# Kernel tuning notes

Measured on AMD Instinct MI355X. Metric: run time of the kernel, lower is better.

## Reference

```python
import jax, jax.numpy as jnp
import numpy as np

B, N, D = 8, 256, 128
EPS_AGG = 1e-6
LN_EPS = 1e-5


def setup_inputs() -> dict:
    key = jax.random.key(0)
    ks = jax.random.split(key, 12)
    s = lambda fan_in: 1.0 / np.sqrt(fan_in)
    inp = {
        "x": jax.random.normal(ks[0], (B, N, D), dtype=jnp.float32),
        "edge0": jax.random.normal(ks[1], (B, N, N, D), dtype=jnp.float32),
        "edge_mask": jax.random.randint(ks[2], (B, N, N), 0, 2, dtype=jnp.int32),
        # msg_mlp: Linear(3D->D), ReLU, Linear(D->D)
        "W1m": jax.random.uniform(ks[3], (3 * D, D), jnp.float32, -s(3 * D), s(3 * D)),
        "b1m": jax.random.uniform(ks[4], (D,), jnp.float32, -s(3 * D), s(3 * D)),
        "W2m": jax.random.uniform(ks[5], (D, D), jnp.float32, -s(D), s(D)),
        "b2m": jax.random.uniform(ks[6], (D,), jnp.float32, -s(D), s(D)),
        # upd_mlp: Linear(2D->D), ReLU, Linear(D->D)
        "W1u": jax.random.uniform(ks[7], (2 * D, D), jnp.float32, -s(2 * D), s(2 * D)),
        "b1u": jax.random.uniform(ks[8], (D,), jnp.float32, -s(2 * D), s(2 * D)),
        "W2u": jax.random.uniform(ks[9], (D, D), jnp.float32, -s(D), s(D)),
        "b2u": jax.random.uniform(ks[10], (D,), jnp.float32, -s(D), s(D)),
        # LayerNorm affine
        "gamma": jnp.ones((D,), jnp.float32),
        "beta": jnp.zeros((D,), jnp.float32),
    }
    return inp


def reference(x, edge0, edge_mask, W1m, b1m, W2m, b2m, W1u, b1u, W2u, b2u, gamma, beta):
    # All-pairs concat: [B, N_i, N_j, 3D]
    xi = jnp.broadcast_to(x[:, :, None, :], (B, N, N, D))
    xj = jnp.broadcast_to(x[:, None, :, :], (B, N, N, D))
    msg_in = jnp.concatenate([xi, xj, edge0], axis=-1)
    # 2-layer edge MLP
    h = jax.nn.relu(jnp.einsum("bijk,kd->bijd", msg_in, W1m) + b1m)
    msg = jnp.einsum("bijk,kd->bijd", h, W2m) + b2m
    # mask + mean-style aggregation over neighbors j
    m = edge_mask.astype(jnp.float32)
    agg = jnp.einsum("bijd,bij->bid", msg, m) / (m.sum(axis=2, keepdims=True) + EPS_AGG)
    # update MLP
    u_in = jnp.concatenate([x, agg], axis=-1)  # [B, N, 2D]
    hu = jax.nn.relu(u_in @ W1u + b1u)
    out = hu @ W2u + b2u
    # residual + LayerNorm
    y = x + out
    mu = y.mean(axis=-1, keepdims=True)
    var = y.var(axis=-1, keepdims=True)
    return (y - mu) * jax.lax.rsqrt(var + LN_EPS) * gamma + beta
```

## Files before the change

kernel.cpp:

```cpp
#include <hip/hip_runtime.h>
#include <hip/hip_bf16.h>

typedef float    f4    __attribute__((ext_vector_type(4)));
typedef short    s8v   __attribute__((ext_vector_type(8)));
typedef __bf16   bf8v  __attribute__((ext_vector_type(8)));
typedef unsigned int u32x4v __attribute__((ext_vector_type(4)));
typedef unsigned short u16;

typedef const __attribute__((address_space(1))) void GAS;
typedef __attribute__((address_space(3))) void LAS;

#define NB 8
#define NN 256
#define ND 128

static __device__ __forceinline__ u16 f2bf(float f) {
    union { float f; unsigned u; } v; v.f = f;
    unsigned r = v.u + 0x7FFF + ((v.u >> 16) & 1);
    return (u16)(r >> 16);
}

static __device__ __forceinline__ unsigned pack2bf(float a, float b) {
    unsigned ua = __builtin_bit_cast(unsigned, a) + 0x8000u;
    unsigned ub = __builtin_bit_cast(unsigned, b) + 0x8000u;
    return __builtin_amdgcn_perm(ub, ua, 0x07060302u);
}

__global__ __launch_bounds__(256) void prep_kernel(
    const float* __restrict__ x, const float* __restrict__ W1m,
    const float* __restrict__ b1m,
    float* __restrict__ P, float* __restrict__ Qt, u16* __restrict__ W1cp)
{
    if (blockIdx.x == 1024) {
        for (int idx = threadIdx.x; idx < 16384; idx += 256) {
            int e  = idx & 7;
            int ln = (idx >> 3) & 63;
            int nt = (idx >> 9) & 7;
            int kt = idx >> 12;
            int k  = kt * 32 + (ln >> 4) * 8 + e;
            int d  = nt * 16 + (ln & 15);
            W1cp[idx] = f2bf(W1m[(2 * ND + k) * ND + d]);
        }
        return;
    }
    __shared__ float xl[256];
    int t = threadIdx.x;
    int row0 = blockIdx.x * 2;
    xl[t] = x[row0 * ND + t];
    __syncthreads();
    int r = t >> 7;
    int d = t & 127;
    int row = row0 + r;
    float sp = b1m[d], sq = 0.f;
    const float* xr = &xl[r * ND];
    #pragma unroll 8
    for (int k = 0; k < ND; ++k) {
        float xv = xr[k];
        sp += xv * W1m[k * ND + d];
        sq += xv * W1m[(ND + k) * ND + d];
    }
    P[row * ND + d] = sp;
    Qt[((size_t)((row >> 8) * ND + d)) * NN + (row & 255)] = sq;
}

__global__ __launch_bounds__(256, 4) void fused_kernel(
    const float* __restrict__ x, const float* __restrict__ edge0,
    const int* __restrict__ mask,
    const float* __restrict__ W2m, const float* __restrict__ b2m,
    const float* __restrict__ W1u, const float* __restrict__ b1u,
    const float* __restrict__ W2u, const float* __restrict__ b2u,
    const float* __restrict__ gamma, const float* __restrict__ beta,
    const float* __restrict__ P, const float* __restrict__ Qt,
    const u16* __restrict__ W1cp,
    float* __restrict__ out)
{
    __shared__ float ebuf[2][32 * 128];
    __shared__ float ml[NN];
    __shared__ float aggH[ND];
    __shared__ float xrow[ND];
    __shared__ float am[ND];
    __shared__ float hu[ND];
    __shared__ float yl[ND];
    __shared__ float redc[4], redA[4], redB[4];

    const int bid  = blockIdx.x;
    const int b    = bid >> 8;
    const int tid  = threadIdx.x;
    const int wave = tid >> 6;
    const int lane = tid & 63;
    const int l15  = lane & 15;
    const int lg   = lane >> 4;

    const char* e0c = (const char*)(edge0 + (size_t)bid * (NN * ND));

    float mval = (float)mask[bid * NN + tid];
    ml[tid] = mval;
    if (tid < ND) xrow[tid] = x[bid * ND + tid];

    s8v bfr[4][2];
    #pragma unroll
    for (int kt = 0; kt < 4; ++kt)
        #pragma unroll
        for (int n = 0; n < 2; ++n)
            bfr[kt][n] = *reinterpret_cast<const s8v*>(
                &W1cp[(((kt * 8) + (wave * 2 + n)) * 64 + lane) * 8]);

    const int col0 = wave * 32 + l15;
    const float pv0 = P[bid * ND + col0];
    const float pv1 = P[bid * ND + col0 + 16];
    const float* qt0 = Qt + (size_t)(b * ND + col0) * NN;
    const float* qt1 = qt0 + (size_t)16 * NN;

    auto STAGE = [&](int cc, int bb) {
        const char* cb = e0c + (size_t)cc * 16384;
        #pragma unroll
        for (int u = 0; u < 4; ++u) {
            int row  = wave * 8 + u * 2 + (lane >> 5);
            int colb = (lane & 31) * 16;
            const char* g = cb + row * 512 + (colb ^ ((row & 7) << 4));
            __builtin_amdgcn_global_load_lds(
                (GAS*)g, (LAS*)&ebuf[bb][(wave * 4 + u) * 256], 16, 0, 0);
        }
    };

    float agg0 = 0.f, agg1 = 0.f;
    f4 q0r[2][2], q1r[2][2];

    #pragma unroll
    for (int m = 0; m < 2; ++m) {
        int j0 = m * 16 + lg * 4;
        q0r[0][m] = *reinterpret_cast<const f4*>(qt0 + j0);
        q1r[0][m] = *reinterpret_cast<const f4*>(qt1 + j0);
    }
    __builtin_amdgcn_sched_barrier(0);
    STAGE(0, 0);
    __builtin_amdgcn_sched_barrier(0);

    #pragma unroll
    for (int c = 0; c < 8; ++c) {
        const int pb = c & 1, nb = pb ^ 1;
        if (c < 7) {
            #pragma unroll
            for (int m = 0; m < 2; ++m) {
                int j0 = (c + 1) * 32 + m * 16 + lg * 4;
                q0r[nb][m] = *reinterpret_cast<const f4*>(qt0 + j0);
                q1r[nb][m] = *reinterpret_cast<const f4*>(qt1 + j0);
            }
            __builtin_amdgcn_sched_barrier(0);
            STAGE(c + 1, nb);
            __builtin_amdgcn_sched_barrier(0);
            asm volatile("s_waitcnt vmcnt(8) lgkmcnt(0)" ::: "memory");
        } else {
            asm volatile("s_waitcnt vmcnt(0) lgkmcnt(0)" ::: "memory");
        }
        __builtin_amdgcn_s_barrier();
        __builtin_amdgcn_sched_barrier(0);

        const char* bufc = (const char*)&ebuf[pb][0];
        #pragma unroll
        for (int m = 0; m < 2; ++m) {
            f4 acc0 = {0.f, 0.f, 0.f, 0.f};
            f4 acc1 = {0.f, 0.f, 0.f, 0.f};
            int row = m * 16 + l15;
            int rb  = row * 512;
            int swz = (row & 7) << 4;
            #pragma unroll
            for (int kt = 0; kt < 4; ++kt) {
                int cbyte = kt * 128 + lg * 32;
                f4 a0 = *reinterpret_cast<const f4*>(bufc + rb + ((cbyte)      ^ swz));
                f4 a1 = *reinterpret_cast<const f4*>(bufc + rb + ((cbyte + 16) ^ swz));
                u32x4v aw;
                aw[0] = pack2bf(a0[0], a0[1]);
                aw[1] = pack2bf(a0[2], a0[3]);
                aw[2] = pack2bf(a1[0], a1[1]);
                aw[3] = pack2bf(a1[2], a1[3]);
                bf8v av = __builtin_bit_cast(bf8v, aw);
                acc0 = __builtin_amdgcn_mfma_f32_16x16x32_bf16(
                    av, __builtin_bit_cast(bf8v, bfr[kt][0]), acc0, 0, 0, 0);
                acc1 = __builtin_amdgcn_mfma_f32_16x16x32_bf16(
                    av, __builtin_bit_cast(bf8v, bfr[kt][1]), acc1, 0, 0, 0);
            }
            int j0 = c * 32 + m * 16 + lg * 4;
            f4 q0 = q0r[pb][m];
            f4 q1 = q1r[pb][m];
            #pragma unroll
            for (int r = 0; r < 4; ++r) {
                float mm = ml[j0 + r];
                float h0 = fmaxf(acc0[r] + pv0 + q0[r], 0.f);
                float h1 = fmaxf(acc1[r] + pv1 + q1[r], 0.f);
                agg0 += mm * h0;
                agg1 += mm * h1;
            }
        }
        __builtin_amdgcn_sched_barrier(0);
        __builtin_amdgcn_s_barrier();
    }

    agg0 += __shfl_xor(agg0, 16); agg0 += __shfl_xor(agg0, 32);
    agg1 += __shfl_xor(agg1, 16); agg1 += __shfl_xor(agg1, 32);
    if (lg == 0) {
        aggH[wave * 32 + l15]      = agg0;
        aggH[wave * 32 + 16 + l15] = agg1;
    }
    float cv = mval;
    #pragma unroll
    for (int o = 32; o > 0; o >>= 1) cv += __shfl_xor(cv, o);
    if (lane == 0) redc[wave] = cv;
    __syncthreads();

    const float cnt = redc[0] + redc[1] + redc[2] + redc[3];
    const float inv = 1.f / (cnt + 1e-6f);
    const int d  = tid & 127;
    const int hf = tid >> 7;

    {
        float s = 0.f;
        #pragma unroll 8
        for (int k = hf * 64; k < hf * 64 + 64; ++k) s += aggH[k] * W2m[k * ND + d];
        ml[tid] = s;
    }
    __syncthreads();
    if (tid < ND) am[d] = (ml[d] + ml[d + ND] + cnt * b2m[d]) * inv;
    __syncthreads();
    {
        float s = 0.f;
        const float* W = W1u + (size_t)hf * ND * ND;
        const float* v = hf ? am : xrow;
        #pragma unroll 8
        for (int k = 0; k < ND; ++k) s += v[k] * W[k * ND + d];
        ml[tid] = s;
    }
    __syncthreads();
    if (tid < ND) hu[d] = fmaxf(ml[d] + ml[d + ND] + b1u[d], 0.f);
    __syncthreads();
    {
        float s = 0.f;
        #pragma unroll 8
        for (int k = hf * 64; k < hf * 64 + 64; ++k) s += hu[k] * W2u[k * ND + d];
        ml[tid] = s;
    }
    __syncthreads();
    if (tid < ND) yl[d] = xrow[d] + ml[d] + ml[d + ND] + b2u[d];
    __syncthreads();
    float yv = (tid < ND) ? yl[tid] : 0.f;
    float s1 = yv, s2 = yv * yv;
    #pragma unroll
    for (int o = 32; o > 0; o >>= 1) { s1 += __shfl_xor(s1, o); s2 += __shfl_xor(s2, o); }
    if (lane == 0) { redA[wave] = s1; redB[wave] = s2; }
    __syncthreads();
    if (tid < ND) {
        float mu  = (redA[0] + redA[1] + redA[2] + redA[3]) * (1.f / 128.f);
        float ex2 = (redB[0] + redB[1] + redB[2] + redB[3]) * (1.f / 128.f);
        float var = ex2 - mu * mu;
        float rs  = rsqrtf(var + 1e-5f);
        out[bid * ND + d] = (yl[d] - mu) * rs * gamma[d] + beta[d];
    }
}

extern "C" void kernel_launch(void* const* d_in, const int* in_sizes, int n_in,
                              void* d_out, int out_size, void* d_ws, size_t ws_size,
                              hipStream_t stream) {
    (void)in_sizes; (void)n_in; (void)out_size; (void)ws_size;
    const float* x     = (const float*)d_in[0];
    const float* edge0 = (const float*)d_in[1];
    const int*   mask  = (const int*)d_in[2];
    const float* W1m   = (const float*)d_in[3];
    const float* b1m   = (const float*)d_in[4];
    const float* W2m   = (const float*)d_in[5];
    const float* b2m   = (const float*)d_in[6];
    const float* W1u   = (const float*)d_in[7];
    const float* b1u   = (const float*)d_in[8];
    const float* W2u   = (const float*)d_in[9];
    const float* b2u   = (const float*)d_in[10];
    const float* gamma = (const float*)d_in[11];
    const float* beta  = (const float*)d_in[12];

    float* P    = (float*)d_ws;
    float* Qt   = P + 2048 * 128;
    u16*   W1cp = (u16*)(Qt + 8 * 128 * 256);

    float* o = (float*)d_out;

    prep_kernel<<<dim3(1025), dim3(256), 0, stream>>>(x, W1m, b1m, P, Qt, W1cp);
    fused_kernel<<<dim3(2048), dim3(256), 0, stream>>>(
        x, edge0, mask, W2m, b2m, W1u, b1u, W2u, b2u, gamma, beta,
        P, Qt, W1cp, o);
}
```

Before: 101.0 us.

## Triple-buffer edge staging and drop per-iteration trailing barrier

Switches the edge tile staging from double to triple buffering, prefetching two chunks ahead and issuing the next loads right after the top barrier. This removes the second block-wide barrier per iteration and deepens load latency hiding. Epilogue shared arrays are aliased onto the first staging buffer to limit LDS growth, and launch bounds are lowered to 3 blocks per CU to match the larger LDS footprint, trading occupancy for pipelining depth.

```diff
diff --git a/kernel.cpp b/kernel.cpp
--- a/kernel.cpp
+++ b/kernel.cpp
@@ -63,7 +63,7 @@
     Qt[((size_t)((row >> 8) * ND + d)) * NN + (row & 255)] = sq;
 }
 
-__global__ __launch_bounds__(256, 4) void fused_kernel(
+__global__ __launch_bounds__(256, 3) void fused_kernel(
     const float* __restrict__ x, const float* __restrict__ edge0,
     const int* __restrict__ mask,
     const float* __restrict__ W2m, const float* __restrict__ b2m,
@@ -74,14 +74,15 @@
     const u16* __restrict__ W1cp,
     float* __restrict__ out)
 {
-    __shared__ float ebuf[2][32 * 128];
+    __shared__ float ebuf[3][32 * 128];
     __shared__ float ml[NN];
-    __shared__ float aggH[ND];
     __shared__ float xrow[ND];
-    __shared__ float am[ND];
-    __shared__ float hu[ND];
-    __shared__ float yl[ND];
     __shared__ float redc[4], redA[4], redB[4];
+
+    float* aggH = &ebuf[0][0];
+    float* am   = &ebuf[0][128];
+    float* hu   = &ebuf[0][256];
+    float* yl   = &ebuf[0][384];
 
     const int bid  = blockIdx.x;
     const int b    = bid >> 8;
@@ -124,39 +125,42 @@
     };
 
     float agg0 = 0.f, agg1 = 0.f;
-    f4 q0r[2][2], q1r[2][2];
-
-    #pragma unroll
-    for (int m = 0; m < 2; ++m) {
-        int j0 = m * 16 + lg * 4;
-        q0r[0][m] = *reinterpret_cast<const f4*>(qt0 + j0);
-        q1r[0][m] = *reinterpret_cast<const f4*>(qt1 + j0);
-    }
+    f4 q0r[3][2], q1r[3][2];
+
+    auto LOADQ = [&](int cc, int gg) {
+        #pragma unroll
+        for (int m = 0; m < 2; ++m) {
+            int j0 = cc * 32 + m * 16 + lg * 4;
+            q0r[gg][m] = *reinterpret_cast<const f4*>(qt0 + j0);
+            q1r[gg][m] = *reinterpret_cast<const f4*>(qt1 + j0);
+        }
+    };
+
+    LOADQ(0, 0);
     __builtin_amdgcn_sched_barrier(0);
     STAGE(0, 0);
     __builtin_amdgcn_sched_barrier(0);
+    LOADQ(1, 1);
+    __builtin_amdgcn_sched_barrier(0);
+    STAGE(1, 1);
+    __builtin_amdgcn_sched_barrier(0);
 
     #pragma unroll
     for (int c = 0; c < 8; ++c) {
-        const int pb = c & 1, nb = pb ^ 1;
-        if (c < 7) {
-            #pragma unroll
-            for (int m = 0; m < 2; ++m) {
-                int j0 = (c + 1) * 32 + m * 16 + lg * 4;
-                q0r[nb][m] = *reinterpret_cast<const f4*>(qt0 + j0);
-                q1r[nb][m] = *reinterpret_cast<const f4*>(qt1 + j0);
-            }
-            __builtin_amdgcn_sched_barrier(0);
-            STAGE(c + 1, nb);
-            __builtin_amdgcn_sched_barrier(0);
+        const int g = c % 3;
+        if (c < 7)
             asm volatile("s_waitcnt vmcnt(8) lgkmcnt(0)" ::: "memory");
-        } else {
+        else
             asm volatile("s_waitcnt vmcnt(0) lgkmcnt(0)" ::: "memory");
-        }
         __builtin_amdgcn_s_barrier();
         __builtin_amdgcn_sched_barrier(0);
-
-        const char* bufc = (const char*)&ebuf[pb][0];
+        if (c < 6) {
+            LOADQ(c + 2, (c + 2) % 3);
+            __builtin_amdgcn_sched_barrier(0);
+            STAGE(c + 2, (c + 2) % 3);
+            __builtin_amdgcn_sched_barrier(0);
+        }
+        const char* bufc = (const char*)&ebuf[g][0];
         #pragma unroll
         for (int m = 0; m < 2; ++m) {
             f4 acc0 = {0.f, 0.f, 0.f, 0.f};
@@ -181,8 +185,8 @@
                     av, __builtin_bit_cast(bf8v, bfr[kt][1]), acc1, 0, 0, 0);
             }
             int j0 = c * 32 + m * 16 + lg * 4;
-            f4 q0 = q0r[pb][m];
-            f4 q1 = q1r[pb][m];
+            f4 q0 = q0r[g][m];
+            f4 q1 = q1r[g][m];
             #pragma unroll
             for (int r = 0; r < 4; ++r) {
                 float mm = ml[j0 + r];
@@ -192,8 +196,6 @@
                 agg1 += mm * h1;
             }
         }
-        __builtin_amdgcn_sched_barrier(0);
-        __builtin_amdgcn_s_barrier();
     }
 
     agg0 += __shfl_xor(agg0, 16); agg0 += __shfl_xor(agg0, 32);
```

Result: slower. 107.1 us (+6.0%).

## Compute xj projection via MFMA from staged bf16 x instead of precomputed Qt

Applied to the files above, without the earlier changes.

Drops the precomputed fp32 Qt (x_j·W1m middle block) and instead stages a bf16 copy of x alongside each edge tile in LDS, adding a second set of MFMAs per tile that multiply it by bf16 W1m weights. This removes the per-chunk Qt register loads and the scalar prep GEMM for Q, in exchange for doubling MFMA work and enlarging LDS. LDS is cut back by aliasing the small epilogue arrays into ebuf, and occupancy is lowered to 3 blocks. Block IDs are remapped so that consecutive blocks land in different batches, which spreads the xbf reads. The x_j term now runs in bf16 rather than fp32, so accuracy is slightly lower.

```diff
diff --git a/kernel.cpp b/kernel.cpp
--- a/kernel.cpp
+++ b/kernel.cpp
@@ -29,17 +29,20 @@
 __global__ __launch_bounds__(256) void prep_kernel(
     const float* __restrict__ x, const float* __restrict__ W1m,
     const float* __restrict__ b1m,
-    float* __restrict__ P, float* __restrict__ Qt, u16* __restrict__ W1cp)
+    float* __restrict__ P, u16* __restrict__ xbf_g, u16* __restrict__ W1cp)
 {
     if (blockIdx.x == 1024) {
-        for (int idx = threadIdx.x; idx < 16384; idx += 256) {
-            int e  = idx & 7;
-            int ln = (idx >> 3) & 63;
-            int nt = (idx >> 9) & 7;
-            int kt = idx >> 12;
+        for (int idx = threadIdx.x; idx < 32768; idx += 256) {
+            int half = idx >> 14;
+            int r  = idx & 16383;
+            int e  = r & 7;
+            int ln = (r >> 3) & 63;
+            int nt = (r >> 9) & 7;
+            int kt = r >> 12;
             int k  = kt * 32 + (ln >> 4) * 8 + e;
             int d  = nt * 16 + (ln & 15);
-            W1cp[idx] = f2bf(W1m[(2 * ND + k) * ND + d]);
+            int krow = half ? (ND + k) : (2 * ND + k);
+            W1cp[idx] = f2bf(W1m[krow * ND + d]);
         }
         return;
     }
@@ -51,39 +54,36 @@
     int r = t >> 7;
     int d = t & 127;
     int row = row0 + r;
-    float sp = b1m[d], sq = 0.f;
+    float sp = b1m[d];
     const float* xr = &xl[r * ND];
     #pragma unroll 8
-    for (int k = 0; k < ND; ++k) {
-        float xv = xr[k];
-        sp += xv * W1m[k * ND + d];
-        sq += xv * W1m[(ND + k) * ND + d];
-    }
+    for (int k = 0; k < ND; ++k) sp += xr[k] * W1m[k * ND + d];
     P[row * ND + d] = sp;
-    Qt[((size_t)((row >> 8) * ND + d)) * NN + (row & 255)] = sq;
-}
-
-__global__ __launch_bounds__(256, 4) void fused_kernel(
+    xbf_g[row * ND + d] = f2bf(xr[d]);
+}
+
+__global__ __launch_bounds__(256, 3) void fused_kernel(
     const float* __restrict__ x, const float* __restrict__ edge0,
     const int* __restrict__ mask,
     const float* __restrict__ W2m, const float* __restrict__ b2m,
     const float* __restrict__ W1u, const float* __restrict__ b1u,
     const float* __restrict__ W2u, const float* __restrict__ b2u,
     const float* __restrict__ gamma, const float* __restrict__ beta,
-    const float* __restrict__ P, const float* __restrict__ Qt,
+    const float* __restrict__ P, const u16* __restrict__ xbf_g,
     const u16* __restrict__ W1cp,
     float* __restrict__ out)
 {
-    __shared__ float ebuf[2][32 * 128];
+    __shared__ float ebuf[2][6144];
     __shared__ float ml[NN];
-    __shared__ float aggH[ND];
     __shared__ float xrow[ND];
-    __shared__ float am[ND];
-    __shared__ float hu[ND];
-    __shared__ float yl[ND];
     __shared__ float redc[4], redA[4], redB[4];
 
-    const int bid  = blockIdx.x;
+    float* aggH = &ebuf[0][0];
+    float* am   = &ebuf[0][128];
+    float* hu   = &ebuf[0][256];
+    float* yl   = &ebuf[0][384];
+
+    const int bid  = (blockIdx.x & 7) * 256 + (blockIdx.x >> 3);
     const int b    = bid >> 8;
     const int tid  = threadIdx.x;
     const int wave = tid >> 6;
@@ -92,24 +92,25 @@
     const int lg   = lane >> 4;
 
     const char* e0c = (const char*)(edge0 + (size_t)bid * (NN * ND));
+    const char* xbc = (const char*)(xbf_g + (size_t)b * NN * ND);
 
     float mval = (float)mask[bid * NN + tid];
     ml[tid] = mval;
     if (tid < ND) xrow[tid] = x[bid * ND + tid];
 
-    s8v bfr[4][2];
+    s8v bfrC[4][2], bfrB[4][2];
     #pragma unroll
     for (int kt = 0; kt < 4; ++kt)
         #pragma unroll
-        for (int n = 0; n < 2; ++n)
-            bfr[kt][n] = *reinterpret_cast<const s8v*>(
-                &W1cp[(((kt * 8) + (wave * 2 + n)) * 64 + lane) * 8]);
+        for (int n = 0; n < 2; ++n) {
+            int fo = (((kt * 8) + (wave * 2 + n)) * 64 + lane) * 8;
+            bfrC[kt][n] = *reinterpret_cast<const s8v*>(&W1cp[fo]);
+            bfrB[kt][n] = *reinterpret_cast<const s8v*>(&W1cp[16384 + fo]);
+        }
 
     const int col0 = wave * 32 + l15;
     const float pv0 = P[bid * ND + col0];
     const float pv1 = P[bid * ND + col0 + 16];
-    const float* qt0 = Qt + (size_t)(b * ND + col0) * NN;
-    const float* qt1 = qt0 + (size_t)16 * NN;
 
     auto STAGE = [&](int cc, int bb) {
         const char* cb = e0c + (size_t)cc * 16384;
@@ -121,18 +122,19 @@
             __builtin_amdgcn_global_load_lds(
                 (GAS*)g, (LAS*)&ebuf[bb][(wave * 4 + u) * 256], 16, 0, 0);
         }
+        const char* xb = xbc + (size_t)cc * 8192;
+        #pragma unroll
+        for (int u = 0; u < 2; ++u) {
+            int row  = wave * 8 + u * 4 + (lane >> 4);
+            int colb = (lane & 15) * 16;
+            const char* g = xb + row * 256 + (colb ^ ((row & 7) << 4));
+            __builtin_amdgcn_global_load_lds(
+                (GAS*)g, (LAS*)&ebuf[bb][4096 + (wave * 2 + u) * 256], 16, 0, 0);
+        }
     };
 
     float agg0 = 0.f, agg1 = 0.f;
-    f4 q0r[2][2], q1r[2][2];
-
-    #pragma unroll
-    for (int m = 0; m < 2; ++m) {
-        int j0 = m * 16 + lg * 4;
-        q0r[0][m] = *reinterpret_cast<const f4*>(qt0 + j0);
-        q1r[0][m] = *reinterpret_cast<const f4*>(qt1 + j0);
-    }
-    __builtin_amdgcn_sched_barrier(0);
+
     STAGE(0, 0);
     __builtin_amdgcn_sched_barrier(0);
 
@@ -140,16 +142,9 @@
     for (int c = 0; c < 8; ++c) {
         const int pb = c & 1, nb = pb ^ 1;
         if (c < 7) {
-            #pragma unroll
-            for (int m = 0; m < 2; ++m) {
-                int j0 = (c + 1) * 32 + m * 16 + lg * 4;
-                q0r[nb][m] = *reinterpret_cast<const f4*>(qt0 + j0);
-                q1r[nb][m] = *reinterpret_cast<const f4*>(qt1 + j0);
-            }
-            __builtin_amdgcn_sched_barrier(0);
             STAGE(c + 1, nb);
             __builtin_amdgcn_sched_barrier(0);
-            asm volatile("s_waitcnt vmcnt(8) lgkmcnt(0)" ::: "memory");
+            asm volatile("s_waitcnt vmcnt(6) lgkmcnt(0)" ::: "memory");
         } else {
             asm volatile("s_waitcnt vmcnt(0) lgkmcnt(0)" ::: "memory");
         }
@@ -176,18 +171,25 @@
                 aw[3] = pack2bf(a1[2], a1[3]);
                 bf8v av = __builtin_bit_cast(bf8v, aw);
                 acc0 = __builtin_amdgcn_mfma_f32_16x16x32_bf16(
-                    av, __builtin_bit_cast(bf8v, bfr[kt][0]), acc0, 0, 0, 0);
+                    av, __builtin_bit_cast(bf8v, bfrC[kt][0]), acc0, 0, 0, 0);
                 acc1 = __builtin_amdgcn_mfma_f32_16x16x32_bf16(
-                    av, __builtin_bit_cast(bf8v, bfr[kt][1]), acc1, 0, 0, 0);
+                    av, __builtin_bit_cast(bf8v, bfrC[kt][1]), acc1, 0, 0, 0);
+            }
+            #pragma unroll
+            for (int kt = 0; kt < 4; ++kt) {
+                int xoffb = 16384 + row * 256 + ((kt * 64 + lg * 16) ^ swz);
+                s8v xa = *reinterpret_cast<const s8v*>(bufc + xoffb);
+                acc0 = __builtin_amdgcn_mfma_f32_16x16x32_bf16(
+                    __builtin_bit_cast(bf8v, xa), __builtin_bit_cast(bf8v, bfrB[kt][0]), acc0, 0, 0, 0);
+                acc1 = __builtin_amdgcn_mfma_f32_16x16x32_bf16(
+                    __builtin_bit_cast(bf8v, xa), __builtin_bit_cast(bf8v, bfrB[kt][1]), acc1, 0, 0, 0);
             }
             int j0 = c * 32 + m * 16 + lg * 4;
-            f4 q0 = q0r[pb][m];
-            f4 q1 = q1r[pb][m];
             #pragma unroll
             for (int r = 0; r < 4; ++r) {
                 float mm = ml[j0 + r];
-                float h0 = fmaxf(acc0[r] + pv0 + q0[r], 0.f);
-                float h1 = fmaxf(acc1[r] + pv1 + q1[r], 0.f);
+                float h0 = fmaxf(acc0[r] + pv0, 0.f);
+                float h1 = fmaxf(acc1[r] + pv1, 0.f);
                 agg0 += mm * h0;
                 agg1 += mm * h1;
             }
@@ -276,13 +278,13 @@
     const float* beta  = (const float*)d_in[12];
 
     float* P    = (float*)d_ws;
-    float* Qt   = P + 2048 * 128;
-    u16*   W1cp = (u16*)(Qt + 8 * 128 * 256);
+    u16*   xbf  = (u16*)(P + 2048 * 128);
+    u16*   W1cp = xbf + 2048 * 128;
 
     float* o = (float*)d_out;
 
-    prep_kernel<<<dim3(1025), dim3(256), 0, stream>>>(x, W1m, b1m, P, Qt, W1cp);
+    prep_kernel<<<dim3(1025), dim3(256), 0, stream>>>(x, W1m, b1m, P, xbf, W1cp);
     fused_kernel<<<dim3(2048), dim3(256), 0, stream>>>(
         x, edge0, mask, W2m, b2m, W1u, b1u, W2u, b2u, gamma, beta,
-        P, Qt, W1cp, o);
-}
+        P, xbf, W1cp, o);
+}
```

Result: slower. 114.4 us (+13.2%).

## Split neighbor rows across waves with per-wave LDS buffers and full-width B fragments

Applied to the files above, without the earlier changes.

Each wave now owns 64 neighbor rows and computes all 128 output columns, holding the full W1 edge-slice B fragments (32 registers of 8 bf16) in registers. Each wave streams its own double-buffered LDS tile, so the per-chunk block barriers go away, and the A fragment is packed once and reused across 8 MFMA column tiles. The per-wave partial aggregates are then summed through LDS. Block indices are also remapped so consecutive blocks come from different batches, and launch bounds are lowered to 2 blocks per CU because register use and LDS use grow.

```diff
diff --git a/kernel.cpp b/kernel.cpp
--- a/kernel.cpp
+++ b/kernel.cpp
@@ -63,7 +63,7 @@
     Qt[((size_t)((row >> 8) * ND + d)) * NN + (row & 255)] = sq;
 }
 
-__global__ __launch_bounds__(256, 4) void fused_kernel(
+__global__ __launch_bounds__(256, 2) void fused_kernel(
     const float* __restrict__ x, const float* __restrict__ edge0,
     const int* __restrict__ mask,
     const float* __restrict__ W2m, const float* __restrict__ b2m,
@@ -74,16 +74,12 @@
     const u16* __restrict__ W1cp,
     float* __restrict__ out)
 {
-    __shared__ float ebuf[2][32 * 128];
+    __shared__ float ebuf[4][2][2048];
     __shared__ float ml[NN];
-    __shared__ float aggH[ND];
     __shared__ float xrow[ND];
-    __shared__ float am[ND];
-    __shared__ float hu[ND];
-    __shared__ float yl[ND];
     __shared__ float redc[4], redA[4], redB[4];
 
-    const int bid  = blockIdx.x;
+    const int bid  = (blockIdx.x & 7) * 256 + (blockIdx.x >> 3);
     const int b    = bid >> 8;
     const int tid  = threadIdx.x;
     const int wave = tid >> 6;
@@ -91,127 +87,123 @@
     const int l15  = lane & 15;
     const int lg   = lane >> 4;
 
-    const char* e0c = (const char*)(edge0 + (size_t)bid * (NN * ND));
+    const char* e0c = (const char*)(edge0 + (size_t)bid * (NN * ND))
+                    + (size_t)wave * 64 * 512;
 
     float mval = (float)mask[bid * NN + tid];
     ml[tid] = mval;
     if (tid < ND) xrow[tid] = x[bid * ND + tid];
 
-    s8v bfr[4][2];
+    s8v bfr[4][8];
     #pragma unroll
     for (int kt = 0; kt < 4; ++kt)
         #pragma unroll
-        for (int n = 0; n < 2; ++n)
-            bfr[kt][n] = *reinterpret_cast<const s8v*>(
-                &W1cp[(((kt * 8) + (wave * 2 + n)) * 64 + lane) * 8]);
-
-    const int col0 = wave * 32 + l15;
-    const float pv0 = P[bid * ND + col0];
-    const float pv1 = P[bid * ND + col0 + 16];
-    const float* qt0 = Qt + (size_t)(b * ND + col0) * NN;
-    const float* qt1 = qt0 + (size_t)16 * NN;
-
-    auto STAGE = [&](int cc, int bb) {
-        const char* cb = e0c + (size_t)cc * 16384;
-        #pragma unroll
-        for (int u = 0; u < 4; ++u) {
-            int row  = wave * 8 + u * 2 + (lane >> 5);
+        for (int nt = 0; nt < 8; ++nt)
+            bfr[kt][nt] = *reinterpret_cast<const s8v*>(
+                &W1cp[(((kt * 8) + nt) * 64 + lane) * 8]);
+
+    float pv[8];
+    #pragma unroll
+    for (int nt = 0; nt < 8; ++nt) pv[nt] = P[bid * ND + nt * 16 + l15];
+
+    const float* qb = Qt + ((size_t)b * ND + l15) * NN + wave * 64 + lg * 4;
+
+    float agg[8] = {0.f, 0.f, 0.f, 0.f, 0.f, 0.f, 0.f, 0.f};
+
+    auto STAGE = [&](int t, int bb) {
+        const char* cb = e0c + (size_t)t * 8192;
+        #pragma unroll
+        for (int u = 0; u < 8; ++u) {
+            int row  = u * 2 + (lane >> 5);
             int colb = (lane & 31) * 16;
             const char* g = cb + row * 512 + (colb ^ ((row & 7) << 4));
             __builtin_amdgcn_global_load_lds(
-                (GAS*)g, (LAS*)&ebuf[bb][(wave * 4 + u) * 256], 16, 0, 0);
+                (GAS*)g, (LAS*)&ebuf[wave][bb][u * 256], 16, 0, 0);
         }
     };
 
-    float agg0 = 0.f, agg1 = 0.f;
-    f4 q0r[2][2], q1r[2][2];
-
-    #pragma unroll
-    for (int m = 0; m < 2; ++m) {
-        int j0 = m * 16 + lg * 4;
-        q0r[0][m] = *reinterpret_cast<const f4*>(qt0 + j0);
-        q1r[0][m] = *reinterpret_cast<const f4*>(qt1 + j0);
-    }
+    asm volatile("s_waitcnt vmcnt(0) lgkmcnt(0)" ::: "memory");
     __builtin_amdgcn_sched_barrier(0);
     STAGE(0, 0);
     __builtin_amdgcn_sched_barrier(0);
 
     #pragma unroll
-    for (int c = 0; c < 8; ++c) {
-        const int pb = c & 1, nb = pb ^ 1;
-        if (c < 7) {
+    for (int t = 0; t < 4; ++t) {
+        const int pb = t & 1;
+        f4 qv[8];
+        #pragma unroll
+        for (int nt = 0; nt < 8; ++nt)
+            qv[nt] = *reinterpret_cast<const f4*>(qb + nt * 4096 + t * 16);
+        __builtin_amdgcn_sched_barrier(0);
+        if (t < 3) {
+            STAGE(t + 1, pb ^ 1);
+            __builtin_amdgcn_sched_barrier(0);
+            asm volatile("s_waitcnt vmcnt(8)" ::: "memory");
+        } else {
+            asm volatile("s_waitcnt vmcnt(0)" ::: "memory");
+        }
+        __builtin_amdgcn_sched_barrier(0);
+
+        f4 mk = *reinterpret_cast<const f4*>(&ml[wave * 64 + t * 16 + lg * 4]);
+
+        const char* bufc = (const char*)&ebuf[wave][pb][0];
+        const int rb  = l15 * 512;
+        const int swz = (l15 & 7) << 4;
+        s8v apk[4];
+        #pragma unroll
+        for (int kt = 0; kt < 4; ++kt) {
+            int cbyte = kt * 128 + lg * 32;
+            f4 a0 = *reinterpret_cast<const f4*>(bufc + rb + ((cbyte)      ^ swz));
+            f4 a1 = *reinterpret_cast<const f4*>(bufc + rb + ((cbyte + 16) ^ swz));
+            u32x4v aw;
+            aw[0] = pack2bf(a0[0], a0[1]);
+            aw[1] = pack2bf(a0[2], a0[3]);
+            aw[2] = pack2bf(a1[0], a1[1]);
+            aw[3] = pack2bf(a1[2], a1[3]);
+            apk[kt] = __builtin_bit_cast(s8v, aw);
+        }
+        #pragma unroll
+        for (int nt = 0; nt < 8; ++nt) {
+            f4 acc = {0.f, 0.f, 0.f, 0.f};
             #pragma unroll
-            for (int m = 0; m < 2; ++m) {
-                int j0 = (c + 1) * 32 + m * 16 + lg * 4;
-                q0r[nb][m] = *reinterpret_cast<const f4*>(qt0 + j0);
-                q1r[nb][m] = *reinterpret_cast<const f4*>(qt1 + j0);
-            }
-            __builtin_amdgcn_sched_barrier(0);
-            STAGE(c + 1, nb);
-            __builtin_amdgcn_sched_barrier(0);
-            asm volatile("s_waitcnt vmcnt(8) lgkmcnt(0)" ::: "memory");
-        } else {
-            asm volatile("s_waitcnt vmcnt(0) lgkmcnt(0)" ::: "memory");
-        }
-        __builtin_amdgcn_s_barrier();
-        __builtin_amdgcn_sched_barrier(0);
-
-        const char* bufc = (const char*)&ebuf[pb][0];
-        #pragma unroll
-        for (int m = 0; m < 2; ++m) {
-            f4 acc0 = {0.f, 0.f, 0.f, 0.f};
-            f4 acc1 = {0.f, 0.f, 0.f, 0.f};
-            int row = m * 16 + l15;
-            int rb  = row * 512;
-            int swz = (row & 7) << 4;
-            #pragma unroll
-            for (int kt = 0; kt < 4; ++kt) {
-                int cbyte = kt * 128 + lg * 32;
-                f4 a0 = *reinterpret_cast<const f4*>(bufc + rb + ((cbyte)      ^ swz));
-                f4 a1 = *reinterpret_cast<const f4*>(bufc + rb + ((cbyte + 16) ^ swz));
-                u32x4v aw;
-                aw[0] = pack2bf(a0[0], a0[1]);
-                aw[1] = pack2bf(a0[2], a0[3]);
-                aw[2] = pack2bf(a1[0], a1[1]);
-                aw[3] = pack2bf(a1[2], a1[3]);
-                bf8v av = __builtin_bit_cast(bf8v, aw);
-                acc0 = __builtin_amdgcn_mfma_f32_16x16x32_bf16(
-                    av, __builtin_bit_cast(bf8v, bfr[kt][0]), acc0, 0, 0, 0);
-                acc1 = __builtin_amdgcn_mfma_f32_16x16x32_bf16(
-                    av, __builtin_bit_cast(bf8v, bfr[kt][1]), acc1, 0, 0, 0);
-            }
-            int j0 = c * 32 + m * 16 + lg * 4;
-            f4 q0 = q0r[pb][m];
-            f4 q1 = q1r[pb][m];
+            for (int kt = 0; kt < 4; ++kt)
+                acc = __builtin_amdgcn_mfma_f32_16x16x32_bf16(
+                    __builtin_bit_cast(bf8v, apk[kt]),
+                    __builtin_bit_cast(bf8v, bfr[kt][nt]), acc, 0, 0, 0);
             #pragma unroll
             for (int r = 0; r < 4; ++r) {
-                float mm = ml[j0 + r];
-                float h0 = fmaxf(acc0[r] + pv0 + q0[r], 0.f);
-                float h1 = fmaxf(acc1[r] + pv1 + q1[r], 0.f);
-                agg0 += mm * h0;
-                agg1 += mm * h1;
+                float h = fmaxf(acc[r] + pv[nt] + qv[nt][r], 0.f);
+                agg[nt] += mk[r] * h;
             }
         }
-        __builtin_amdgcn_sched_barrier(0);
-        __builtin_amdgcn_s_barrier();
-    }
-
-    agg0 += __shfl_xor(agg0, 16); agg0 += __shfl_xor(agg0, 32);
-    agg1 += __shfl_xor(agg1, 16); agg1 += __shfl_xor(agg1, 32);
-    if (lg == 0) {
-        aggH[wave * 32 + l15]      = agg0;
-        aggH[wave * 32 + 16 + l15] = agg1;
+    }
+
+    #pragma unroll
+    for (int nt = 0; nt < 8; ++nt) {
+        float a = agg[nt];
+        a += __shfl_xor(a, 16);
+        a += __shfl_xor(a, 32);
+        if (lg == 0) ebuf[wave][0][nt * 16 + l15] = a;
     }
     float cv = mval;
     #pragma unroll
     for (int o = 32; o > 0; o >>= 1) cv += __shfl_xor(cv, o);
     if (lane == 0) redc[wave] = cv;
     __syncthreads();
+
+    float* aggH = &ebuf[0][1][1024];
+    float* am   = &ebuf[1][1][1024];
+    float* hu   = &ebuf[2][1][1024];
+    float* yl   = &ebuf[3][1][1024];
 
     const float cnt = redc[0] + redc[1] + redc[2] + redc[3];
     const float inv = 1.f / (cnt + 1e-6f);
     const int d  = tid & 127;
     const int hf = tid >> 7;
+
+    if (tid < ND)
+        aggH[tid] = ebuf[0][0][tid] + ebuf[1][0][tid] + ebuf[2][0][tid] + ebuf[3][0][tid];
+    __syncthreads();
 
     {
         float s = 0.f;
```

Measured after the change: 229.7 us. +127.4%, slower.
